# Optimization experiments

Hardware: AMD Instinct MI355X
Metric: run time of the kernel (lower is better)

The kernel has to match this reference:

```python
import jax, jax.numpy as jnp
import numpy as np

N_HEADS = 12
ROPE_THETA = 10000.0


def _rope(x):
    # x: [B, L, N, D]; interleaved (lucidrains rotary_embedding_torch style) rotation over full D
    B, L, N, D = x.shape
    inv_freq = 1.0 / (ROPE_THETA ** (jnp.arange(0, D, 2, dtype=jnp.float32) / D))  # [D/2]
    freqs = jnp.arange(L, dtype=jnp.float32)[:, None] * inv_freq                    # [L, D/2]
    cos = jnp.repeat(jnp.cos(freqs), 2, axis=-1)[None, :, None, :].astype(x.dtype)  # [1,L,1,D]
    sin = jnp.repeat(jnp.sin(freqs), 2, axis=-1)[None, :, None, :].astype(x.dtype)
    x1 = x[..., 0::2]
    x2 = x[..., 1::2]
    x_rot = jnp.stack([-x2, x1], axis=-1).reshape(x.shape)  # rotate_half, interleaved pairs
    return x * cos + x_rot * sin


def setup_inputs() -> dict:
    key = jax.random.key(0)
    ks = jax.random.split(key, 7)
    B, L, dm = 8, 1024, 768
    x = jax.random.normal(ks[0], (B, L, dm), jnp.float32)
    mask = jax.random.randint(ks[1], (B, L), 0, 2, jnp.int32)          # 1 = keep, 0 = pad
    pos_bias = jax.random.normal(ks[2], (N_HEADS, L, L), jnp.float32) * 0.1
    qkv_w = jax.random.normal(ks[3], (3 * dm, dm), jnp.float32) * 0.02
    qkv_b = jax.random.normal(ks[4], (3 * dm,), jnp.float32) * 0.02
    out_w = jax.random.normal(ks[5], (dm, dm), jnp.float32) * 0.02
    out_b = jax.random.normal(ks[6], (dm,), jnp.float32) * 0.02
    return {"x": x, "pos_bias": pos_bias, "qkv_w": qkv_w, "qkv_b": qkv_b,
            "out_w": out_w, "out_b": out_b, "mask": mask}


def reference(x, pos_bias, qkv_w, qkv_b, out_w, out_b, mask):
    B, L, dm = x.shape
    N = N_HEADS
    D = dm // N
    # QKV projection (torch Linear: y = x @ W.T + b), chunk(3, -1)
    qkv = x @ qkv_w.T + qkv_b                                   # [B, L, 3*dm]
    q, k, v = [a.reshape(B, L, N, D) for a in jnp.split(qkv, 3, axis=-1)]
    q = _rope(q)
    k = _rope(k)
    # scores [B, N, Lq, Lk]
    scores = jnp.einsum('bqnd,bknd->bnqk', q, k) / jnp.sqrt(jnp.asarray(D, x.dtype))
    # mask_to_bias: (mask - 1) with negatives -> -inf, shape [B, 1, 1, L]
    mask_bias = jnp.where(mask > 0, 0.0, -jnp.inf).astype(x.dtype)[:, None, None, :]
    bias = pos_bias[None].astype(x.dtype) + mask_bias           # [B, N, L, L]
    attn = jax.nn.softmax(scores + bias, axis=-1)               # dropout = 0 (eval)
    o = jnp.einsum('bnqk,bknd->bqnd', attn, v).reshape(B, L, dm)
    return o @ out_w.T + out_b
```

## Files before the change

### kernel.cpp

```cpp
#include <hip/hip_runtime.h>

#define DEVINL __device__ __forceinline__

using bf16x8 = __attribute__((ext_vector_type(8))) short;
using f32x4  = __attribute__((ext_vector_type(4))) float;

constexpr int Bb = 8, Ls = 1024, DM = 768, NH = 12, DH = 64;
constexpr int QKV = 3 * DM;

DEVINL unsigned short f2bf(float f) {
    union { float f; unsigned u; } v; v.f = f;
    unsigned r = v.u + 0x7FFFu + ((v.u >> 16) & 1u);
    return (unsigned short)(r >> 16);
}
DEVINL float bf2f(unsigned short h) {
    union { unsigned u; float f; } v; v.u = ((unsigned)h) << 16; return v.f;
}

DEVINL void gload_lds16(const void* g, void* l) {
    __builtin_amdgcn_global_load_lds((const __attribute__((address_space(1))) void*)g,
                                     (__attribute__((address_space(3))) void*)l, 16, 0, 0);
}

__global__ void prep_kernel(const float* __restrict__ x, const float* __restrict__ wq,
                            const float* __restrict__ wo, const float* __restrict__ pbias,
                            unsigned short* __restrict__ xb, unsigned short* __restrict__ wqb,
                            unsigned short* __restrict__ wob, unsigned short* __restrict__ ebb,
                            float* __restrict__ tab) {
    const int X4 = Bb * Ls * DM / 4, W4 = QKV * DM / 4, O4 = DM * DM / 4;
    const int E4 = NH * Ls * Ls / 4, TB = Ls * DH;
    const int total = X4 + W4 + O4 + E4 + TB;
    for (int idx = blockIdx.x * blockDim.x + threadIdx.x; idx < total;
         idx += gridDim.x * blockDim.x) {
        if (idx < X4 + W4 + O4) {
            const float4* s; unsigned short* d; int i;
            if (idx < X4)            { s = (const float4*)x;  d = xb;  i = idx; }
            else if (idx < X4 + W4)  { s = (const float4*)wq; d = wqb; i = idx - X4; }
            else                     { s = (const float4*)wo; d = wob; i = idx - X4 - W4; }
            float4 v = s[i];
            ushort4 o;
            o.x = f2bf(v.x); o.y = f2bf(v.y); o.z = f2bf(v.z); o.w = f2bf(v.w);
            ((ushort4*)d)[i] = o;
        } else if (idx < X4 + W4 + O4 + E4) {
            int i = idx - (X4 + W4 + O4);
            float4 v = ((const float4*)pbias)[i];
            ushort4 o;
            o.x = f2bf(__expf(v.x)); o.y = f2bf(__expf(v.y));
            o.z = f2bf(__expf(v.z)); o.w = f2bf(__expf(v.w));
            ((ushort4*)ebb)[i] = o;
        } else {
            int r = idx - (X4 + W4 + O4 + E4);
            int l = r >> 6, c = r & 63, i = c & 31;
            float freq = powf(10000.0f, -(float)i / 32.0f);
            float ang = (float)l * freq;
            tab[l * 64 + c] = (c < 32) ? cosf(ang) : sinf(ang);
        }
    }
}

template <int OUT_BF16>
__global__ __launch_bounds__(256) void gemm_nt(const unsigned short* __restrict__ A,
                                               const unsigned short* __restrict__ Bw,
                                               const float* __restrict__ bias,
                                               void* __restrict__ Cout,
                                               int M, int Nn, int K) {
    __shared__ unsigned short As[2][128 * 32];
    __shared__ unsigned short Bs[2][128 * 32];
    const int tid = threadIdx.x, lane = tid & 63, w = tid >> 6;
    const int bm = blockIdx.x * 128, bn = blockIdx.y * 128;
    const int wm = w >> 1, wn = w & 1;
    const int col = lane & 15, q4 = lane >> 4;
    f32x4 acc[4][4] = {};

#define GSTAGE(bi, kt_)                                                              \
    {                                                                                \
        _Pragma("unroll") for (int i = 0; i < 2; ++i) {                              \
            int c0 = w * 128 + i * 64;                                               \
            int p = c0 + lane;                                                       \
            int row = p >> 2;                                                        \
            int kc = (p & 3) ^ (row & 3);                                            \
            gload_lds16(A + (size_t)(bm + row) * K + (kt_)*32 + kc * 8, &As[bi][c0 * 8]); \
            gload_lds16(Bw + (size_t)(bn + row) * K + (kt_)*32 + kc * 8, &Bs[bi][c0 * 8]); \
        }                                                                            \
    }

    const int NT = K / 32;
    GSTAGE(0, 0);
    for (int t = 0; t < NT; ++t) {
        const int cur = t & 1;
        if (t + 1 < NT) {
            GSTAGE(cur ^ 1, t + 1);
            asm volatile("s_waitcnt vmcnt(4)" ::: "memory");
        } else {
            asm volatile("s_waitcnt vmcnt(0)" ::: "memory");
        }
        __builtin_amdgcn_s_barrier();
        asm volatile("" ::: "memory");
        bf16x8 af[4], bfr[4];
#pragma unroll
        for (int tt = 0; tt < 4; ++tt) {
            int ra = wm * 64 + tt * 16 + col;
            int rb = wn * 64 + tt * 16 + col;
            af[tt]  = *(const bf16x8*)&As[cur][(ra * 32 + q4 * 8) ^ ((ra & 3) << 3)];
            bfr[tt] = *(const bf16x8*)&Bs[cur][(rb * 32 + q4 * 8) ^ ((rb & 3) << 3)];
        }
#pragma unroll
        for (int tt = 0; tt < 4; ++tt)
#pragma unroll
            for (int u = 0; u < 4; ++u)
                acc[tt][u] = __builtin_amdgcn_mfma_f32_16x16x32_bf16(af[tt], bfr[u], acc[tt][u], 0, 0, 0);
        __builtin_amdgcn_sched_barrier(0);
        asm volatile("" ::: "memory");
        __builtin_amdgcn_s_barrier();
    }
#undef GSTAGE
#pragma unroll
    for (int t = 0; t < 4; ++t) {
        int grow_base = bm + wm * 64 + t * 16 + q4 * 4;
#pragma unroll
        for (int u = 0; u < 4; ++u) {
            int gcol = bn + wn * 64 + u * 16 + col;
            float bv = bias[gcol];
#pragma unroll
            for (int r = 0; r < 4; ++r) {
                float vv = acc[t][u][r] + bv;
                if (OUT_BF16)
                    ((unsigned short*)Cout)[(size_t)(grow_base + r) * Nn + gcol] = f2bf(vv);
                else
                    ((float*)Cout)[(size_t)(grow_base + r) * Nn + gcol] = vv;
            }
        }
    }
}

__global__ void rope_qk(const unsigned short* __restrict__ qkvb, const float* __restrict__ tab,
                        unsigned short* __restrict__ qs, unsigned short* __restrict__ ks) {
    const int b = blockIdx.z, n = blockIdx.y;
    const int idx = blockIdx.x * blockDim.x + threadIdx.x;
    const int l = idx >> 3, d8 = idx & 7;
    const float QSCL = 0.125f * 1.44269504089f;
    const unsigned short* src = qkvb + (size_t)(b * Ls + l) * QKV + n * DH + d8 * 8;
    float4 cs = *(const float4*)&tab[l * 64 + d8 * 4];
    float4 sn = *(const float4*)&tab[l * 64 + 32 + d8 * 4];
    float cv[4] = {cs.x, cs.y, cs.z, cs.w};
    float sv[4] = {sn.x, sn.y, sn.z, sn.w};
    size_t dsto = ((size_t)(b * NH + n) * Ls + l) * DH + d8 * 8;
    {
        bf16x8 qv = *(const bf16x8*)src;
        bf16x8 ov;
#pragma unroll
        for (int j = 0; j < 4; ++j) {
            float x1 = bf2f((unsigned short)qv[2 * j]), x2 = bf2f((unsigned short)qv[2 * j + 1]);
            ov[2 * j]     = (short)f2bf((x1 * cv[j] - x2 * sv[j]) * QSCL);
            ov[2 * j + 1] = (short)f2bf((x2 * cv[j] + x1 * sv[j]) * QSCL);
        }
        *(bf16x8*)(qs + dsto) = ov;
    }
    {
        bf16x8 kv = *(const bf16x8*)(src + DM);
        bf16x8 ov;
#pragma unroll
        for (int j = 0; j < 4; ++j) {
            float x1 = bf2f((unsigned short)kv[2 * j]), x2 = bf2f((unsigned short)kv[2 * j + 1]);
            ov[2 * j]     = (short)f2bf(x1 * cv[j] - x2 * sv[j]);
            ov[2 * j + 1] = (short)f2bf(x2 * cv[j] + x1 * sv[j]);
        }
        *(bf16x8*)(ks + dsto) = ov;
    }
}

__global__ void vtrans(const unsigned short* __restrict__ qkvb, unsigned short* __restrict__ vt) {
    __shared__ unsigned short vsh[64][72];
    const int b = blockIdx.z, n = blockIdx.y, lt = blockIdx.x;
    const int tid = threadIdx.x;
#pragma unroll
    for (int i = 0; i < 2; ++i) {
        int c = tid + i * 256;
        int lrow = c >> 3, d8 = c & 7;
        *(bf16x8*)&vsh[lrow][d8 * 8] =
            *(const bf16x8*)(qkvb + (size_t)(b * Ls + lt * 64 + lrow) * QKV + 2 * DM + n * DH + d8 * 8);
    }
    __syncthreads();
#pragma unroll
    for (int i = 0; i < 2; ++i) {
        int c = tid + i * 256;
        int d = c >> 3, l8 = c & 7;
        bf16x8 v;
#pragma unroll
        for (int j = 0; j < 8; ++j) v[j] = (short)vsh[l8 * 8 + j][d];
        *(bf16x8*)(vt + ((size_t)(b * NH + n) * DH + d) * Ls + lt * 64 + l8 * 8) = v;
    }
}

__global__ __launch_bounds__(256) void attn_kernel(const unsigned short* __restrict__ qs,
                                                   const unsigned short* __restrict__ ks,
                                                   const unsigned short* __restrict__ vt,
                                                   const unsigned short* __restrict__ ebb,
                                                   const int* __restrict__ mask,
                                                   unsigned short* __restrict__ ob) {
    __shared__ unsigned short Ksh[2][64 * 64];
    __shared__ unsigned short Vsh[2][64 * 64];
    __shared__ unsigned short EBsh[64 * 64];
    __shared__ unsigned short Psh[4][16 * 64];
    __shared__ float maskb[Ls];
    const int b = blockIdx.x, n = blockIdx.y, qt = blockIdx.z;
    const int tid = threadIdx.x, lane = tid & 63, w = tid >> 6;
    const int col = lane & 15, q4 = lane >> 4;
    for (int i = tid; i < Ls; i += 256)
        maskb[i] = (mask[b * Ls + i] > 0) ? 0.0f : -1e30f;
    const unsigned short* qbn = qs + (size_t)(b * NH + n) * Ls * DH;
    const unsigned short* kbn = ks + (size_t)(b * NH + n) * Ls * DH;
    const unsigned short* vbn = vt + (size_t)(b * NH + n) * DH * Ls;
    const unsigned short* ebn = ebb + (size_t)n * Ls * Ls;
    bf16x8 qf[2];
#pragma unroll
    for (int j = 0; j < 2; ++j)
        qf[j] = *(const bf16x8*)(qbn + (size_t)(qt * 64 + w * 16 + col) * DH + q4 * 8 + j * 32);
    const int qrow_c = w * 16 + q4 * 4;
    float psum[4] = {0.f, 0.f, 0.f, 0.f};
    f32x4 oacc[4];
#pragma unroll
    for (int t = 0; t < 4; ++t) oacc[t] = f32x4{0.f, 0.f, 0.f, 0.f};
    __syncthreads();

#define STAGE_KV(bi, kt_)                                                                  \
    {                                                                                      \
        _Pragma("unroll") for (int i = 0; i < 2; ++i) {                                    \
            int c0 = w * 128 + i * 64;                                                     \
            int p = c0 + lane;                                                             \
            int row = p >> 3, cin = (p & 7) ^ (row & 7);                                   \
            gload_lds16(kbn + (size_t)((kt_)*64 + row) * DH + cin * 8, &Ksh[bi][c0 * 8]);  \
            gload_lds16(vbn + (size_t)row * Ls + (kt_)*64 + cin * 8, &Vsh[bi][c0 * 8]);    \
        }                                                                                  \
    }
#define STAGE_EB(kt_)                                                                      \
    {                                                                                      \
        _Pragma("unroll") for (int i = 0; i < 2; ++i) {                                    \
            int c0 = w * 128 + i * 64;                                                     \
            int p = c0 + lane;                                                             \
            int row = p >> 3, cin = (p & 7) ^ (row & 7);                                   \
            gload_lds16(ebn + (size_t)(qt * 64 + row) * Ls + (kt_)*64 + cin * 8, &EBsh[c0 * 8]); \
        }                                                                                  \
    }

    const int NT = Ls / 64;
    STAGE_KV(0, 0);
    STAGE_EB(0);
    for (int kt = 0; kt < NT; ++kt) {
        const int cur = kt & 1;
        if (kt + 1 < NT) {
            STAGE_KV(cur ^ 1, kt + 1);
            asm volatile("s_waitcnt vmcnt(4)" ::: "memory");
        } else {
            asm volatile("s_waitcnt vmcnt(0)" ::: "memory");
        }
        __builtin_amdgcn_s_barrier();
        asm volatile("" ::: "memory");
        f32x4 s[4];
#pragma unroll
        for (int t = 0; t < 4; ++t) {
            s[t] = f32x4{0.f, 0.f, 0.f, 0.f};
            int krow = t * 16 + col;
#pragma unroll
            for (int j = 0; j < 2; ++j) {
                bf16x8 kf = *(const bf16x8*)&Ksh[cur][(krow * 64 + q4 * 8 + j * 32) ^ ((krow & 7) << 3)];
                s[t] = __builtin_amdgcn_mfma_f32_16x16x32_bf16(qf[j], kf, s[t], 0, 0, 0);
            }
        }
        float p[4][4];
#pragma unroll
        for (int t = 0; t < 4; ++t) {
            int kg = kt * 64 + t * 16 + col;
            float ma = maskb[kg];
            int chunk = t * 2 + (col >> 3);
#pragma unroll
            for (int r = 0; r < 4; ++r) {
                int rowl = qrow_c + r;
                int bo = rowl * 128 + (((chunk ^ (rowl & 7)) << 4)) + ((col & 7) << 1);
                float ebf = bf2f(*(const unsigned short*)((const char*)EBsh + bo));
                float pv = exp2f(s[t][r] + ma) * ebf;
                p[t][r] = pv;
                psum[r] += pv;
            }
        }
        asm volatile("s_waitcnt lgkmcnt(0)" ::: "memory");
        __builtin_amdgcn_sched_barrier(0);
        if (kt + 1 < NT) STAGE_EB(kt + 1);
        unsigned short* pw = Psh[w];
#pragma unroll
        for (int t = 0; t < 4; ++t)
#pragma unroll
            for (int r = 0; r < 4; ++r) {
                int row = q4 * 4 + r;
                pw[(row * 64 + t * 16 + col) ^ ((row & 7) << 3)] = f2bf(p[t][r]);
            }
#pragma unroll
        for (int ot = 0; ot < 4; ++ot) {
            int vrow = ot * 16 + col;
#pragma unroll
            for (int j = 0; j < 2; ++j) {
                bf16x8 pa = *(const bf16x8*)&pw[(col * 64 + q4 * 8 + j * 32) ^ ((col & 7) << 3)];
                bf16x8 vb = *(const bf16x8*)&Vsh[cur][(vrow * 64 + q4 * 8 + j * 32) ^ ((vrow & 7) << 3)];
                oacc[ot] = __builtin_amdgcn_mfma_f32_16x16x32_bf16(pa, vb, oacc[ot], 0, 0, 0);
            }
        }
        __builtin_amdgcn_sched_barrier(0);
        asm volatile("" ::: "memory");
        __builtin_amdgcn_s_barrier();
    }
#undef STAGE_KV
#undef STAGE_EB
#pragma unroll
    for (int r = 0; r < 4; ++r)
#pragma unroll
        for (int msk = 1; msk < 16; msk <<= 1)
            psum[r] += __shfl_xor(psum[r], msk);
#pragma unroll
    for (int r = 0; r < 4; ++r) {
        int lg = qt * 64 + qrow_c + r;
        float inv = 1.0f / psum[r];
#pragma unroll
        for (int ot = 0; ot < 4; ++ot)
            ob[(size_t)(b * Ls + lg) * DM + n * DH + ot * 16 + col] = f2bf(oacc[ot][r] * inv);
    }
}

extern "C" void kernel_launch(void* const* d_in, const int* in_sizes, int n_in,
                              void* d_out, int out_size, void* d_ws, size_t ws_size,
                              hipStream_t stream) {
    const float* x     = (const float*)d_in[0];
    const float* posb  = (const float*)d_in[1];
    const float* qkv_w = (const float*)d_in[2];
    const float* qkv_b = (const float*)d_in[3];
    const float* out_w = (const float*)d_in[4];
    const float* out_b = (const float*)d_in[5];
    const int*   mask  = (const int*)d_in[6];
    float* out = (float*)d_out;

    char* wp = (char*)d_ws;
    auto alloc = [&](size_t bytes) {
        char* p = wp;
        wp += (bytes + 255) & ~(size_t)255;
        return p;
    };
    unsigned short* xb   = (unsigned short*)alloc((size_t)Bb * Ls * DM * 2);
    unsigned short* wqb  = (unsigned short*)alloc((size_t)QKV * DM * 2);
    unsigned short* wob  = (unsigned short*)alloc((size_t)DM * DM * 2);
    unsigned short* ebb  = (unsigned short*)alloc((size_t)NH * Ls * Ls * 2);
    float*          tab  = (float*)alloc((size_t)Ls * DH * 4);
    unsigned short* qkvb = (unsigned short*)alloc((size_t)Bb * Ls * QKV * 2);
    unsigned short* qsb  = (unsigned short*)alloc((size_t)Bb * NH * Ls * DH * 2);
    unsigned short* ksb  = (unsigned short*)alloc((size_t)Bb * NH * Ls * DH * 2);
    unsigned short* vtb  = (unsigned short*)alloc((size_t)Bb * NH * DH * Ls * 2);
    unsigned short* obb  = (unsigned short*)alloc((size_t)Bb * Ls * DM * 2);

    prep_kernel<<<dim3(2048), dim3(256), 0, stream>>>(x, qkv_w, out_w, posb, xb, wqb, wob, ebb, tab);
    gemm_nt<1><<<dim3(64, 18), dim3(256), 0, stream>>>(xb, wqb, qkv_b, (void*)qkvb, Bb * Ls, QKV, DM);
    rope_qk<<<dim3(32, NH, Bb), dim3(256), 0, stream>>>(qkvb, tab, qsb, ksb);
    vtrans<<<dim3(16, NH, Bb), dim3(256), 0, stream>>>(qkvb, vtb);
    attn_kernel<<<dim3(Bb, NH, 16), dim3(256), 0, stream>>>(qsb, ksb, vtb, ebb, mask, obb);
    gemm_nt<0><<<dim3(64, 6), dim3(256), 0, stream>>>(obb, wob, out_b, (void*)out, Bb * Ls, DM, DM);
}
```

Measured before the change: 285.5 us.

## Fold bias into score init, transpose score MFMA, fuse rope/vtrans, remap block grids

The positional bias is now stored as a log2-scaled additive term rather than an exponent. It and the mask are preloaded into the score accumulator, so the softmax loop does a single exp2 with no per-element multiply or scattered LDS read. The QK MFMA operands are swapped so each lane holds one query row's values. That allows a single psum per lane, packed bf16 conversion with vectorized P stores, and a hoisted P fragment load. Rope and the V transpose are fused into one kernel, the GEMM and attention grids are flattened with a swizzled block order for cache locality, and s_setprio is added around the MFMA sections. The GEMM remap assumes specific grid sizes, and the changed bias representation changes rounding.

```diff
diff --git a/kernel.cpp b/kernel.cpp
--- a/kernel.cpp
+++ b/kernel.cpp
@@ -30,6 +30,7 @@
     const int X4 = Bb * Ls * DM / 4, W4 = QKV * DM / 4, O4 = DM * DM / 4;
     const int E4 = NH * Ls * Ls / 4, TB = Ls * DH;
     const int total = X4 + W4 + O4 + E4 + TB;
+    const float L2E = 1.44269504089f;
     for (int idx = blockIdx.x * blockDim.x + threadIdx.x; idx < total;
          idx += gridDim.x * blockDim.x) {
         if (idx < X4 + W4 + O4) {
@@ -45,8 +46,8 @@
             int i = idx - (X4 + W4 + O4);
             float4 v = ((const float4*)pbias)[i];
             ushort4 o;
-            o.x = f2bf(__expf(v.x)); o.y = f2bf(__expf(v.y));
-            o.z = f2bf(__expf(v.z)); o.w = f2bf(__expf(v.w));
+            o.x = f2bf(v.x * L2E); o.y = f2bf(v.y * L2E);
+            o.z = f2bf(v.z * L2E); o.w = f2bf(v.w * L2E);
             ((ushort4*)ebb)[i] = o;
         } else {
             int r = idx - (X4 + W4 + O4 + E4);
@@ -67,7 +68,9 @@
     __shared__ unsigned short As[2][128 * 32];
     __shared__ unsigned short Bs[2][128 * 32];
     const int tid = threadIdx.x, lane = tid & 63, w = tid >> 6;
-    const int bm = blockIdx.x * 128, bn = blockIdx.y * 128;
+    const int f = blockIdx.x;
+    const int bm = (8 * (f & 7) + ((f >> 3) & 7)) * 128;
+    const int bn = (f >> 6) * 128;
     const int wm = w >> 1, wn = w & 1;
     const int col = lane & 15, q4 = lane >> 4;
     f32x4 acc[4][4] = {};
@@ -133,46 +136,46 @@
     }
 }
 
-__global__ void rope_qk(const unsigned short* __restrict__ qkvb, const float* __restrict__ tab,
-                        unsigned short* __restrict__ qs, unsigned short* __restrict__ ks) {
-    const int b = blockIdx.z, n = blockIdx.y;
-    const int idx = blockIdx.x * blockDim.x + threadIdx.x;
-    const int l = idx >> 3, d8 = idx & 7;
-    const float QSCL = 0.125f * 1.44269504089f;
-    const unsigned short* src = qkvb + (size_t)(b * Ls + l) * QKV + n * DH + d8 * 8;
-    float4 cs = *(const float4*)&tab[l * 64 + d8 * 4];
-    float4 sn = *(const float4*)&tab[l * 64 + 32 + d8 * 4];
-    float cv[4] = {cs.x, cs.y, cs.z, cs.w};
-    float sv[4] = {sn.x, sn.y, sn.z, sn.w};
-    size_t dsto = ((size_t)(b * NH + n) * Ls + l) * DH + d8 * 8;
-    {
-        bf16x8 qv = *(const bf16x8*)src;
-        bf16x8 ov;
-#pragma unroll
-        for (int j = 0; j < 4; ++j) {
-            float x1 = bf2f((unsigned short)qv[2 * j]), x2 = bf2f((unsigned short)qv[2 * j + 1]);
-            ov[2 * j]     = (short)f2bf((x1 * cv[j] - x2 * sv[j]) * QSCL);
-            ov[2 * j + 1] = (short)f2bf((x2 * cv[j] + x1 * sv[j]) * QSCL);
-        }
-        *(bf16x8*)(qs + dsto) = ov;
-    }
-    {
-        bf16x8 kv = *(const bf16x8*)(src + DM);
-        bf16x8 ov;
-#pragma unroll
-        for (int j = 0; j < 4; ++j) {
-            float x1 = bf2f((unsigned short)kv[2 * j]), x2 = bf2f((unsigned short)kv[2 * j + 1]);
-            ov[2 * j]     = (short)f2bf(x1 * cv[j] - x2 * sv[j]);
-            ov[2 * j + 1] = (short)f2bf(x2 * cv[j] + x1 * sv[j]);
-        }
-        *(bf16x8*)(ks + dsto) = ov;
-    }
-}
-
-__global__ void vtrans(const unsigned short* __restrict__ qkvb, unsigned short* __restrict__ vt) {
+__global__ void ropev_kernel(const unsigned short* __restrict__ qkvb, const float* __restrict__ tab,
+                             unsigned short* __restrict__ qs, unsigned short* __restrict__ ks,
+                             unsigned short* __restrict__ vt) {
     __shared__ unsigned short vsh[64][72];
     const int b = blockIdx.z, n = blockIdx.y, lt = blockIdx.x;
     const int tid = threadIdx.x;
+    const float QSCL = 0.125f * 1.44269504089f;
+#pragma unroll
+    for (int i = 0; i < 2; ++i) {
+        int idx = tid + i * 256;
+        int l = lt * 64 + (idx >> 3), d8 = idx & 7;
+        const unsigned short* src = qkvb + (size_t)(b * Ls + l) * QKV + n * DH + d8 * 8;
+        float4 cs = *(const float4*)&tab[l * 64 + d8 * 4];
+        float4 sn = *(const float4*)&tab[l * 64 + 32 + d8 * 4];
+        float cv[4] = {cs.x, cs.y, cs.z, cs.w};
+        float sv[4] = {sn.x, sn.y, sn.z, sn.w};
+        size_t dsto = ((size_t)(b * NH + n) * Ls + l) * DH + d8 * 8;
+        {
+            bf16x8 qv = *(const bf16x8*)src;
+            bf16x8 ov;
+#pragma unroll
+            for (int j = 0; j < 4; ++j) {
+                float x1 = bf2f((unsigned short)qv[2 * j]), x2 = bf2f((unsigned short)qv[2 * j + 1]);
+                ov[2 * j]     = (short)f2bf((x1 * cv[j] - x2 * sv[j]) * QSCL);
+                ov[2 * j + 1] = (short)f2bf((x2 * cv[j] + x1 * sv[j]) * QSCL);
+            }
+            *(bf16x8*)(qs + dsto) = ov;
+        }
+        {
+            bf16x8 kv = *(const bf16x8*)(src + DM);
+            bf16x8 ov;
+#pragma unroll
+            for (int j = 0; j < 4; ++j) {
+                float x1 = bf2f((unsigned short)kv[2 * j]), x2 = bf2f((unsigned short)kv[2 * j + 1]);
+                ov[2 * j]     = (short)f2bf(x1 * cv[j] - x2 * sv[j]);
+                ov[2 * j + 1] = (short)f2bf(x2 * cv[j] + x1 * sv[j]);
+            }
+            *(bf16x8*)(ks + dsto) = ov;
+        }
+    }
 #pragma unroll
     for (int i = 0; i < 2; ++i) {
         int c = tid + i * 256;
@@ -203,7 +206,9 @@
     __shared__ unsigned short EBsh[64 * 64];
     __shared__ unsigned short Psh[4][16 * 64];
     __shared__ float maskb[Ls];
-    const int b = blockIdx.x, n = blockIdx.y, qt = blockIdx.z;
+    const int f = blockIdx.x;
+    const int b = f / 192, t192 = f % 192;
+    const int n = t192 % 12, qt = t192 / 12;
     const int tid = threadIdx.x, lane = tid & 63, w = tid >> 6;
     const int col = lane & 15, q4 = lane >> 4;
     for (int i = tid; i < Ls; i += 256)
@@ -216,8 +221,7 @@
 #pragma unroll
     for (int j = 0; j < 2; ++j)
         qf[j] = *(const bf16x8*)(qbn + (size_t)(qt * 64 + w * 16 + col) * DH + q4 * 8 + j * 32);
-    const int qrow_c = w * 16 + q4 * 4;
-    float psum[4] = {0.f, 0.f, 0.f, 0.f};
+    float psum = 0.f;
     f32x4 oacc[4];
 #pragma unroll
     for (int t = 0; t < 4; ++t) oacc[t] = f32x4{0.f, 0.f, 0.f, 0.f};
@@ -259,69 +263,79 @@
         f32x4 s[4];
 #pragma unroll
         for (int t = 0; t < 4; ++t) {
-            s[t] = f32x4{0.f, 0.f, 0.f, 0.f};
+            const f32x4 ma = *(const f32x4*)&maskb[kt * 64 + t * 16 + q4 * 4];
+            ushort4 ebv = *(const ushort4*)&EBsh[(w * 16 + col) * 64 +
+                                                (((t * 16 + q4 * 4)) ^ ((col & 7) << 3))];
+            s[t][0] = bf2f(ebv.x) + ma[0];
+            s[t][1] = bf2f(ebv.y) + ma[1];
+            s[t][2] = bf2f(ebv.z) + ma[2];
+            s[t][3] = bf2f(ebv.w) + ma[3];
+        }
+        __builtin_amdgcn_s_setprio(1);
+#pragma unroll
+        for (int t = 0; t < 4; ++t) {
             int krow = t * 16 + col;
 #pragma unroll
             for (int j = 0; j < 2; ++j) {
                 bf16x8 kf = *(const bf16x8*)&Ksh[cur][(krow * 64 + q4 * 8 + j * 32) ^ ((krow & 7) << 3)];
-                s[t] = __builtin_amdgcn_mfma_f32_16x16x32_bf16(qf[j], kf, s[t], 0, 0, 0);
-            }
-        }
+                s[t] = __builtin_amdgcn_mfma_f32_16x16x32_bf16(kf, qf[j], s[t], 0, 0, 0);
+            }
+        }
+        __builtin_amdgcn_s_setprio(0);
         float p[4][4];
 #pragma unroll
-        for (int t = 0; t < 4; ++t) {
-            int kg = kt * 64 + t * 16 + col;
-            float ma = maskb[kg];
-            int chunk = t * 2 + (col >> 3);
+        for (int t = 0; t < 4; ++t)
 #pragma unroll
             for (int r = 0; r < 4; ++r) {
-                int rowl = qrow_c + r;
-                int bo = rowl * 128 + (((chunk ^ (rowl & 7)) << 4)) + ((col & 7) << 1);
-                float ebf = bf2f(*(const unsigned short*)((const char*)EBsh + bo));
-                float pv = exp2f(s[t][r] + ma) * ebf;
+                float pv = exp2f(s[t][r]);
                 p[t][r] = pv;
-                psum[r] += pv;
-            }
-        }
+                psum += pv;
+            }
         asm volatile("s_waitcnt lgkmcnt(0)" ::: "memory");
         __builtin_amdgcn_sched_barrier(0);
         if (kt + 1 < NT) STAGE_EB(kt + 1);
         unsigned short* pw = Psh[w];
 #pragma unroll
-        for (int t = 0; t < 4; ++t)
-#pragma unroll
-            for (int r = 0; r < 4; ++r) {
-                int row = q4 * 4 + r;
-                pw[(row * 64 + t * 16 + col) ^ ((row & 7) << 3)] = f2bf(p[t][r]);
-            }
+        for (int t = 0; t < 4; ++t) {
+            unsigned pk0, pk1;
+            asm("v_cvt_pk_bf16_f32 %0, %1, %2" : "=v"(pk0) : "v"(p[t][0]), "v"(p[t][1]));
+            asm("v_cvt_pk_bf16_f32 %0, %1, %2" : "=v"(pk1) : "v"(p[t][2]), "v"(p[t][3]));
+            uint2 pk; pk.x = pk0; pk.y = pk1;
+            *(uint2*)&pw[(col * 64) + (((t * 16 + q4 * 4)) ^ ((col & 7) << 3))] = pk;
+        }
+        bf16x8 pa[2];
+#pragma unroll
+        for (int ksl = 0; ksl < 2; ++ksl)
+            pa[ksl] = *(const bf16x8*)&pw[(col * 64) + ((ksl * 32 + q4 * 8) ^ ((col & 7) << 3))];
+        __builtin_amdgcn_s_setprio(1);
 #pragma unroll
         for (int ot = 0; ot < 4; ++ot) {
             int vrow = ot * 16 + col;
 #pragma unroll
-            for (int j = 0; j < 2; ++j) {
-                bf16x8 pa = *(const bf16x8*)&pw[(col * 64 + q4 * 8 + j * 32) ^ ((col & 7) << 3)];
-                bf16x8 vb = *(const bf16x8*)&Vsh[cur][(vrow * 64 + q4 * 8 + j * 32) ^ ((vrow & 7) << 3)];
-                oacc[ot] = __builtin_amdgcn_mfma_f32_16x16x32_bf16(pa, vb, oacc[ot], 0, 0, 0);
-            }
-        }
+            for (int ksl = 0; ksl < 2; ++ksl) {
+                bf16x8 vb = *(const bf16x8*)&Vsh[cur][(vrow * 64 + q4 * 8 + ksl * 32) ^ ((vrow & 7) << 3)];
+                oacc[ot] = __builtin_amdgcn_mfma_f32_16x16x32_bf16(pa[ksl], vb, oacc[ot], 0, 0, 0);
+            }
+        }
+        __builtin_amdgcn_s_setprio(0);
         __builtin_amdgcn_sched_barrier(0);
         asm volatile("" ::: "memory");
         __builtin_amdgcn_s_barrier();
     }
 #undef STAGE_KV
 #undef STAGE_EB
+    psum += __shfl_xor(psum, 16);
+    psum += __shfl_xor(psum, 32);
+    float inv[4];
 #pragma unroll
     for (int r = 0; r < 4; ++r)
-#pragma unroll
-        for (int msk = 1; msk < 16; msk <<= 1)
-            psum[r] += __shfl_xor(psum[r], msk);
+        inv[r] = 1.0f / __shfl(psum, q4 * 4 + r);
 #pragma unroll
     for (int r = 0; r < 4; ++r) {
-        int lg = qt * 64 + qrow_c + r;
-        float inv = 1.0f / psum[r];
+        int lg = qt * 64 + w * 16 + q4 * 4 + r;
 #pragma unroll
         for (int ot = 0; ot < 4; ++ot)
-            ob[(size_t)(b * Ls + lg) * DM + n * DH + ot * 16 + col] = f2bf(oacc[ot][r] * inv);
+            ob[(size_t)(b * Ls + lg) * DM + n * DH + ot * 16 + col] = f2bf(oacc[ot][r] * inv[r]);
     }
 }
 
@@ -355,9 +369,8 @@
     unsigned short* obb  = (unsigned short*)alloc((size_t)Bb * Ls * DM * 2);
 
     prep_kernel<<<dim3(2048), dim3(256), 0, stream>>>(x, qkv_w, out_w, posb, xb, wqb, wob, ebb, tab);
-    gemm_nt<1><<<dim3(64, 18), dim3(256), 0, stream>>>(xb, wqb, qkv_b, (void*)qkvb, Bb * Ls, QKV, DM);
-    rope_qk<<<dim3(32, NH, Bb), dim3(256), 0, stream>>>(qkvb, tab, qsb, ksb);
-    vtrans<<<dim3(16, NH, Bb), dim3(256), 0, stream>>>(qkvb, vtb);
-    attn_kernel<<<dim3(Bb, NH, 16), dim3(256), 0, stream>>>(qsb, ksb, vtb, ebb, mask, obb);
-    gemm_nt<0><<<dim3(64, 6), dim3(256), 0, stream>>>(obb, wob, out_b, (void*)out, Bb * Ls, DM, DM);
-}
+    gemm_nt<1><<<dim3(1152), dim3(256), 0, stream>>>(xb, wqb, qkv_b, (void*)qkvb, Bb * Ls, QKV, DM);
+    ropev_kernel<<<dim3(16, NH, Bb), dim3(256), 0, stream>>>(qkvb, tab, qsb, ksb, vtb);
+    attn_kernel<<<dim3(1536), dim3(256), 0, stream>>>(qsb, ksb, vtb, ebb, mask, obb);
+    gemm_nt<0><<<dim3(384), dim3(256), 0, stream>>>(obb, wob, out_b, (void*)out, Bb * Ls, DM, DM);
+}
```

New measurement: 277.1 us. -3.0%, faster.
